# Kernel tuning notes

Measured on AMD Instinct MI355X. Metric: run time of the kernel, lower is better.

The kernel has to match this reference:

```python
import jax, jax.numpy as jnp
import numpy as np

TYPE_PANEL, TYPE_DIALOG, TYPE_CHAR = 1, 2, 3
NUM_ELEMS = 64  # max element index per type (panel count cap per page)
B, S, D = 8, 4096, 768
NPC, NDS = 4, 4  # num_panel_classes, num_dialog_shapes


def setup_inputs() -> dict:
    key = jax.random.key(0)
    ks = jax.random.split(key, 16)
    w = lambda k, shp: jax.random.normal(k, shp, dtype=jnp.float32) * 0.02
    return {
        "element_types": jax.random.randint(ks[0], (B, S), 0, 4, dtype=jnp.int32),
        "element_indices": jax.random.randint(ks[1], (B, S), 0, NUM_ELEMS, dtype=jnp.int32),
        "parent_panel_indices": jax.random.randint(ks[2], (B, S), 0, NUM_ELEMS, dtype=jnp.int32),
        "style_vector": jax.random.normal(ks[3], (B, 4), dtype=jnp.float32),
        "type_emb": w(ks[4], (4, D)),
        "index_emb": w(ks[5], (NUM_ELEMS, D)),
        "parent_emb": w(ks[6], (NUM_ELEMS, D)),
        "style_w": w(ks[7], (4, D)),
        "style_b": jnp.zeros((D,), jnp.float32),
        "ln_g": jnp.ones((D,), jnp.float32),
        "ln_b": jnp.zeros((D,), jnp.float32),
        "panel_w": w(ks[8], (D, NPC + 4)),
        "panel_b": jnp.zeros((NPC + 4,), jnp.float32),
        "dialog_w": w(ks[9], (2 * D, NDS + 4)),
        "dialog_b": jnp.zeros((NDS + 4,), jnp.float32),
        "char_w": w(ks[10], (2 * D, 4)),
        "char_b": jnp.zeros((4,), jnp.float32),
    }


def reference(element_types, element_indices, parent_panel_indices, style_vector,
              type_emb, index_emb, parent_emb, style_w, style_b, ln_g, ln_b,
              panel_w, panel_b, dialog_w, dialog_b, char_w, char_b):
    Bv, Sv = element_types.shape
    # --- TokenLayoutEncoder: embedding sum + style projection + LayerNorm ---
    x = type_emb[element_types] + index_emb[element_indices] + parent_emb[parent_panel_indices]
    x = x + (style_vector @ style_w + style_b)[:, None, :]
    mu = x.mean(-1, keepdims=True)
    var = ((x - mu) ** 2).mean(-1, keepdims=True)
    feats = (x - mu) * jax.lax.rsqrt(var + 1e-5) * ln_g + ln_b  # (B,S,D)

    # --- vectorized _build_parent_remap: orig panel idx -> kept panel order pos ---
    panel_mask = element_types == TYPE_PANEL                      # (B,S)
    kept = (jnp.cumsum(panel_mask, axis=1) - 1).astype(jnp.int32) # order pos of each panel token
    brow = jnp.arange(Bv, dtype=jnp.int32)[:, None]
    col = jnp.where(panel_mask, element_indices, NUM_ELEMS)       # dummy slot for non-panels
    remap = (jnp.full((Bv, NUM_ELEMS + 1), -1, jnp.int32)
             .at[brow, col].max(kept))[:, :NUM_ELEMS]             # (B, NUM_ELEMS)
    # kept panel order pos -> sequence position (for parent feature gather)
    slot = jnp.where(panel_mask, kept, Sv)
    seq_ids = jnp.broadcast_to(jnp.arange(Sv, dtype=jnp.int32), (Bv, Sv))
    pos_table = (jnp.zeros((Bv, Sv + 1), jnp.int32)
                 .at[brow, slot].set(seq_ids))[:, :Sv]            # (B,S)

    # --- parent_pos per token (DIALOG/CHAR only), -1 otherwise ---
    child_mask = (element_types == TYPE_DIALOG) | (element_types == TYPE_CHAR)
    ppos = jnp.where(child_mask,
                     jnp.take_along_axis(remap, parent_panel_indices, axis=1), -1)
    valid = ppos >= 0
    pseq = jnp.take_along_axis(pos_table, jnp.clip(ppos, 0, Sv - 1), axis=1)
    parent_feats = jnp.take_along_axis(feats, pseq[..., None], axis=1)
    parent_feats = parent_feats * valid[..., None].astype(feats.dtype)
    cat = jnp.concatenate([feats, parent_feats], axis=-1)         # (B,S,2D)

    # --- ParallelPredictionHeads, masked per token type ---
    panel_out = (feats @ panel_w + panel_b) * panel_mask[..., None].astype(feats.dtype)
    dmask = ((element_types == TYPE_DIALOG) & valid)[..., None].astype(feats.dtype)
    cmask = ((element_types == TYPE_CHAR) & valid)[..., None].astype(feats.dtype)
    dialog_out = (cat @ dialog_w + dialog_b) * dmask
    char_out = (cat @ char_w + char_b) * cmask
    return panel_out, dialog_out, char_out
```

## Files before the change

### kernel.cpp

```cpp
#include <hip/hip_runtime.h>

#define NB 8
#define NS 4096
#define ND 768

#define WPACK_F4 6528

#define MAIN_LDS_F4 3648

typedef float4 f4;

static __device__ __forceinline__ f4 ld4(const float* __restrict__ p, int i) {
    return ((const f4*)p)[i];
}

static __device__ __forceinline__ void dot4(float& acc, const f4& a, const f4& w) {
    acc = fmaf(a.x, w.x, acc);
    acc = fmaf(a.y, w.y, acc);
    acc = fmaf(a.z, w.z, acc);
    acc = fmaf(a.w, w.w, acc);
}

__global__ __launch_bounds__(256) void lp_pre(
    const int* __restrict__ et, const int* __restrict__ ei,
    const float* __restrict__ sv, const float* __restrict__ sw,
    const float* __restrict__ sb,
    const float* __restrict__ pw, const float* __restrict__ dw,
    const float* __restrict__ cw,
    const float* __restrict__ lng, const float* __restrict__ lnb,
    int* __restrict__ table, int* __restrict__ cnt, int* __restrict__ lists,
    float* __restrict__ sprj, float* __restrict__ wpack)
{
    const int bx = blockIdx.x;
    if (bx < 128) {
        const int lane = threadIdx.x & 63;
        const int t = bx * 256 + threadIdx.x;
        const int b = t >> 12;
        const int s = t & (NS - 1);
        const int type = et[t];
        if (type == 1) atomicMax(&table[b * 64 + ei[t]], s + 1);
        #pragma unroll
        for (int role = 0; role < 3; ++role) {
            const int want = (type == role + 1);
            unsigned long long m = __ballot(want);
            if (want) {
                int ldr = __ffsll(m) - 1;
                int base = 0;
                if (lane == ldr) base = atomicAdd(&cnt[role * 8 + b], (int)__popcll(m));
                base = __shfl(base, ldr, 64);
                int pos = (int)__popcll(m & ((1ull << lane) - 1));
                lists[(role * 8 + b) * 4096 + base + pos] = s;
            }
        }
    } else if (bx < 130) {
        const int lane = threadIdx.x & 63;
        const int b = (bx - 128) * 4 + (threadIdx.x >> 6);
        const float sv0 = sv[b*4+0], sv1 = sv[b*4+1], sv2 = sv[b*4+2], sv3 = sv[b*4+3];
        #pragma unroll
        for (int g = 0; g < 3; ++g) {
            int i = g*64 + lane;
            f4 w0 = ld4(sw, i), w1 = ld4(sw, 192+i), w2 = ld4(sw, 384+i), w3 = ld4(sw, 576+i);
            f4 bb = ld4(sb, i);
            f4 r;
            r.x = bb.x + sv0*w0.x + sv1*w1.x + sv2*w2.x + sv3*w3.x;
            r.y = bb.y + sv0*w0.y + sv1*w1.y + sv2*w2.y + sv3*w3.y;
            r.z = bb.z + sv0*w0.z + sv1*w1.z + sv2*w2.z + sv3*w3.z;
            r.w = bb.w + sv0*w0.w + sv1*w1.w + sv2*w2.w + sv3*w3.w;
            ((f4*)(sprj + b*ND))[i] = r;
        }
    } else {
        const int q = (bx - 130) * 256 + threadIdx.x;
        if (q >= WPACK_F4) return;
        f4 r;
        if (q < 1536) {
            int o = q / 192, i = q - o * 192, d0 = 4 * i;
            r.x = pw[(d0+0)*8 + o];
            r.y = pw[(d0+1)*8 + o];
            r.z = pw[(d0+2)*8 + o];
            r.w = pw[(d0+3)*8 + o];
        } else if (q < 4608) {
            int u = q - 1536;
            int o = u / 384, i = u - o * 384;
            int d0 = (i < 192) ? 4*i : 768 + 4*(i - 192);
            r.x = dw[(d0+0)*8 + o];
            r.y = dw[(d0+1)*8 + o];
            r.z = dw[(d0+2)*8 + o];
            r.w = dw[(d0+3)*8 + o];
        } else if (q < 6144) {
            int u = q - 4608;
            int o = u / 384, i = u - o * 384;
            int d0 = (i < 192) ? 4*i : 768 + 4*(i - 192);
            r.x = cw[(d0+0)*4 + o];
            r.y = cw[(d0+1)*4 + o];
            r.z = cw[(d0+2)*4 + o];
            r.w = cw[(d0+3)*4 + o];
        } else if (q < 6336) {
            r = ld4(lng, q - 6144);
        } else {
            r = ld4(lnb, q - 6336);
        }
        ((f4*)wpack)[q] = r;
    }
}

__global__ __launch_bounds__(256) void lp_parent(
    const int* __restrict__ ei, const int* __restrict__ ppi,
    const float* __restrict__ temb, const float* __restrict__ iemb,
    const float* __restrict__ pemb, const float* __restrict__ lng,
    const float* __restrict__ lnb,
    const int* __restrict__ table, const float* __restrict__ sprj,
    float* __restrict__ pfeat)
{
    const int lane = threadIdx.x & 63;
    const int slot = blockIdx.x * 4 + (threadIdx.x >> 6);
    const int b = slot >> 6;
    const int pp = table[slot] - 1;
    if (pp < 0) return;
    const int ptok = b * NS + pp;
    const int pei = ei[ptok], pppi = ppi[ptok];
    const float* ie = iemb + pei * ND;
    const float* pe = pemb + pppi * ND;
    const float* sp = sprj + b * ND;

    f4 x[3]; float s1 = 0.f, sq = 0.f;
    #pragma unroll
    for (int g = 0; g < 3; ++g) {
        int i = g*64 + lane;
        f4 a = ld4(temb + ND, i), c = ld4(ie, i), d = ld4(pe, i), s = ld4(sp, i);
        f4 v;
        v.x = a.x + c.x + d.x + s.x;
        v.y = a.y + c.y + d.y + s.y;
        v.z = a.z + c.z + d.z + s.z;
        v.w = a.w + c.w + d.w + s.w;
        x[g] = v;
        s1 += v.x + v.y + v.z + v.w;
        sq = fmaf(v.x, v.x, sq);
        sq = fmaf(v.y, v.y, sq);
        sq = fmaf(v.z, v.z, sq);
        sq = fmaf(v.w, v.w, sq);
    }
    #pragma unroll
    for (int k = 32; k >= 1; k >>= 1) {
        s1 += __shfl_xor(s1, k, 64);
        sq += __shfl_xor(sq, k, 64);
    }
    float mu = s1 * (1.f/ND);
    float rs = rsqrtf(sq * (1.f/ND) - mu * mu + 1e-5f);
    float c0 = -mu * rs;
    float* dst = pfeat + (size_t)slot * ND;
    #pragma unroll
    for (int g = 0; g < 3; ++g) {
        int i = g*64 + lane;
        f4 gg = ld4(lng, i), bb = ld4(lnb, i);
        f4 v = x[g], xn;
        xn.x = fmaf(v.x, rs, c0); v.x = fmaf(xn.x, gg.x, bb.x);
        xn.y = fmaf(v.y, rs, c0); v.y = fmaf(xn.y, gg.y, bb.y);
        xn.z = fmaf(v.z, rs, c0); v.z = fmaf(xn.z, gg.z, bb.z);
        xn.w = fmaf(v.w, rs, c0); v.w = fmaf(xn.w, gg.w, bb.w);
        ((f4*)dst)[i] = v;
    }
}

__global__ __launch_bounds__(1024) void lp_main(
    const int* __restrict__ ei, const int* __restrict__ ppi,
    const float* __restrict__ temb, const float* __restrict__ iemb,
    const float* __restrict__ pemb,
    const float* __restrict__ pb, const float* __restrict__ db,
    const float* __restrict__ cb,
    const int* __restrict__ table, const int* __restrict__ cnt,
    const int* __restrict__ lists, const float* __restrict__ sprj,
    const float* __restrict__ wpack, const float* __restrict__ pfeat,
    float* __restrict__ out)
{
    __shared__ f4 S[MAIN_LDS_F4];
    const int tid = threadIdx.x;
    const int lane = tid & 63;
    const int wid = tid >> 6;
    const int bx = blockIdx.x;
    const int b = bx >> 6;
    const int r = bx & 63;

    int role, ridx, nb, wbase, wcnt;
    if (r < 16)      { role = 0; ridx = r;      nb = 16; wbase = 0;    wcnt = 1536; }
    else if (r < 48) { role = 1; ridx = r - 16; nb = 32; wbase = 1536; wcnt = 3072; }
    else             { role = 2; ridx = r - 48; nb = 16; wbase = 4608; wcnt = 1536; }

    const f4* wsrc = (const f4*)wpack;
    for (int i = tid; i < wcnt; i += 1024) S[i] = wsrc[wbase + i];
    if (tid < 384) S[3072 + tid] = wsrc[6144 + tid];
    if (tid < 192) S[3456 + tid] = ((const f4*)(sprj + b * ND))[tid];
    __syncthreads();

    const int n = cnt[role * 8 + b];
    const int* lst = lists + (role * 8 + b) * 4096;
    const int tb = b * NS;
    const int step = nb * 16;
    const float* te = temb + (role + 1) * ND;

    for (int i = ridx * 16 + wid; i < n; i += step) {
        const int s = lst[i];
        const int t = tb + s;
        const int my_ei = ei[t], my_ppi = ppi[t];

        int pp = 0;
        if (role != 0) {
            pp = table[b * 64 + my_ppi] - 1;
            if (pp < 0) continue;
        }

        const float* ie = iemb + my_ei * ND;
        const float* pe = pemb + my_ppi * ND;

        f4 x[3];
        float s1 = 0.f, sq = 0.f;
        #pragma unroll
        for (int g = 0; g < 3; ++g) {
            int ii = g * 64 + lane;
            f4 a = ld4(te, ii), c = ld4(ie, ii), d = ld4(pe, ii);
            f4 sp = S[3456 + ii];
            f4 v;
            v.x = a.x + c.x + d.x + sp.x;
            v.y = a.y + c.y + d.y + sp.y;
            v.z = a.z + c.z + d.z + sp.z;
            v.w = a.w + c.w + d.w + sp.w;
            x[g] = v;
            s1 += v.x + v.y + v.z + v.w;
            sq = fmaf(v.x, v.x, sq);
            sq = fmaf(v.y, v.y, sq);
            sq = fmaf(v.z, v.z, sq);
            sq = fmaf(v.w, v.w, sq);
        }
        #pragma unroll
        for (int k = 32; k >= 1; k >>= 1) {
            s1 += __shfl_xor(s1, k, 64);
            sq += __shfl_xor(sq, k, 64);
        }
        float mu = s1 * (1.f / ND);
        float rs = rsqrtf(sq * (1.f / ND) - mu * mu + 1e-5f);
        float c0 = -mu * rs;
        #pragma unroll
        for (int g = 0; g < 3; ++g) {
            int ii = g * 64 + lane;
            f4 gg = S[3072 + ii], bb = S[3264 + ii];
            f4 v = x[g], xn;
            xn.x = fmaf(v.x, rs, c0); v.x = fmaf(xn.x, gg.x, bb.x);
            xn.y = fmaf(v.y, rs, c0); v.y = fmaf(xn.y, gg.y, bb.y);
            xn.z = fmaf(v.z, rs, c0); v.z = fmaf(xn.z, gg.z, bb.z);
            xn.w = fmaf(v.w, rs, c0); v.w = fmaf(xn.w, gg.w, bb.w);
            x[g] = v;
        }

        if (role == 0) {
            float acc[8];
            #pragma unroll
            for (int o = 0; o < 8; ++o) acc[o] = 0.f;
            #pragma unroll
            for (int g = 0; g < 3; ++g) {
                int ii = g * 64 + lane;
                #pragma unroll
                for (int o = 0; o < 8; ++o)
                    dot4(acc[o], x[g], S[o * 192 + ii]);
            }
            #pragma unroll
            for (int k = 32; k >= 1; k >>= 1) {
                #pragma unroll
                for (int o = 0; o < 8; ++o)
                    acc[o] += __shfl_xor(acc[o], k, 64);
            }
            if (lane == 0) {
                f4 r0, r1;
                r0.x = acc[0] + pb[0]; r0.y = acc[1] + pb[1];
                r0.z = acc[2] + pb[2]; r0.w = acc[3] + pb[3];
                r1.x = acc[4] + pb[4]; r1.y = acc[5] + pb[5];
                r1.z = acc[6] + pb[6]; r1.w = acc[7] + pb[7];
                f4* op = (f4*)(out + (size_t)t * 8);
                op[0] = r0; op[1] = r1;
            }
        } else {
            const float* pfr = pfeat + (size_t)(b * 64 + my_ppi) * ND;
            if (role == 1) {
                float acc[8];
                #pragma unroll
                for (int o = 0; o < 8; ++o) acc[o] = 0.f;
                #pragma unroll
                for (int g = 0; g < 3; ++g) {
                    int ii = g * 64 + lane;
                    #pragma unroll
                    for (int o = 0; o < 8; ++o)
                        dot4(acc[o], x[g], S[o * 384 + ii]);
                }
                #pragma unroll
                for (int g = 0; g < 3; ++g)
                    x[g] = ld4(pfr, g * 64 + lane);
                #pragma unroll
                for (int g = 0; g < 3; ++g) {
                    int ii = g * 64 + lane;
                    #pragma unroll
                    for (int o = 0; o < 8; ++o)
                        dot4(acc[o], x[g], S[o * 384 + 192 + ii]);
                }
                #pragma unroll
                for (int k = 32; k >= 1; k >>= 1) {
                    #pragma unroll
                    for (int o = 0; o < 8; ++o)
                        acc[o] += __shfl_xor(acc[o], k, 64);
                }
                if (lane == 0) {
                    f4 r0, r1;
                    r0.x = acc[0] + db[0]; r0.y = acc[1] + db[1];
                    r0.z = acc[2] + db[2]; r0.w = acc[3] + db[3];
                    r1.x = acc[4] + db[4]; r1.y = acc[5] + db[5];
                    r1.z = acc[6] + db[6]; r1.w = acc[7] + db[7];
                    f4* od = (f4*)(out + (size_t)NB * NS * 8 + (size_t)t * 8);
                    od[0] = r0; od[1] = r1;
                }
            } else {
                float acc[4];
                #pragma unroll
                for (int o = 0; o < 4; ++o) acc[o] = 0.f;
                #pragma unroll
                for (int g = 0; g < 3; ++g) {
                    int ii = g * 64 + lane;
                    #pragma unroll
                    for (int o = 0; o < 4; ++o)
                        dot4(acc[o], x[g], S[o * 384 + ii]);
                }
                #pragma unroll
                for (int g = 0; g < 3; ++g)
                    x[g] = ld4(pfr, g * 64 + lane);
                #pragma unroll
                for (int g = 0; g < 3; ++g) {
                    int ii = g * 64 + lane;
                    #pragma unroll
                    for (int o = 0; o < 4; ++o)
                        dot4(acc[o], x[g], S[o * 384 + 192 + ii]);
                }
                #pragma unroll
                for (int k = 32; k >= 1; k >>= 1) {
                    #pragma unroll
                    for (int o = 0; o < 4; ++o)
                        acc[o] += __shfl_xor(acc[o], k, 64);
                }
                if (lane == 0) {
                    f4 r0;
                    r0.x = acc[0] + cb[0]; r0.y = acc[1] + cb[1];
                    r0.z = acc[2] + cb[2]; r0.w = acc[3] + cb[3];
                    ((f4*)(out + (size_t)NB * NS * 16 + (size_t)t * 4))[0] = r0;
                }
            }
        }
    }
}

extern "C" void kernel_launch(void* const* d_in, const int* in_sizes, int n_in,
                              void* d_out, int out_size, void* d_ws, size_t ws_size,
                              hipStream_t stream) {
    const int* et  = (const int*)d_in[0];
    const int* ei  = (const int*)d_in[1];
    const int* ppi = (const int*)d_in[2];
    const float* sv   = (const float*)d_in[3];
    const float* temb = (const float*)d_in[4];
    const float* iemb = (const float*)d_in[5];
    const float* pemb = (const float*)d_in[6];
    const float* sw   = (const float*)d_in[7];
    const float* sb   = (const float*)d_in[8];
    const float* lng  = (const float*)d_in[9];
    const float* lnb  = (const float*)d_in[10];
    const float* pw   = (const float*)d_in[11];
    const float* pb   = (const float*)d_in[12];
    const float* dw   = (const float*)d_in[13];
    const float* db   = (const float*)d_in[14];
    const float* cw   = (const float*)d_in[15];
    const float* cbp  = (const float*)d_in[16];
    float* out = (float*)d_out;

    int*   table = (int*)d_ws;
    int*   cnt   = (int*)((char*)d_ws + 2048);
    float* sprj  = (float*)((char*)d_ws + 4096);
    float* wpack = (float*)((char*)d_ws + 32768);
    int*   lists = (int*)((char*)d_ws + 137216);
    float* pfeat = (float*)((char*)d_ws + 532480);

    hipMemsetAsync(d_ws, 0, 2144, stream);
    hipMemsetAsync(d_out, 0, out_size, stream);

    lp_pre<<<156, 256, 0, stream>>>(et, ei, sv, sw, sb, pw, dw, cw, lng, lnb,
                                    table, cnt, lists, sprj, wpack);
    lp_parent<<<128, 256, 0, stream>>>(ei, ppi, temb, iemb, pemb, lng, lnb,
                                       table, sprj, pfeat);
    lp_main<<<512, 1024, 0, stream>>>(ei, ppi, temb, iemb, pemb,
                                      pb, db, cbp,
                                      table, cnt, lists, sprj, wpack, pfeat,
                                      out);
}
```

Baseline: 152.1 us.

## Replace compacted per-role token lists with direct strided token scan in main kernel

Drops the ballot/atomic list compaction and per-role counters in the pre-pass. The main kernel now scans tokens directly: each block pair owns a contiguous chunk of 128 tokens, one block handling panel and char tokens and the other dialog tokens, with the next token's metadata prefetched. The table is initialised to -1 with memset and stores the raw position, which removes the off-by-one encoding. This cuts atomics and list traffic, but waves now idle on tokens that belong to the other role, so load balance depends on the type mix.

Measured after the change: 139.8 us. 8.1% less time.

```diff
diff --git a/kernel.cpp b/kernel.cpp
--- a/kernel.cpp
+++ b/kernel.cpp
@@ -28,29 +28,15 @@
     const float* __restrict__ pw, const float* __restrict__ dw,
     const float* __restrict__ cw,
     const float* __restrict__ lng, const float* __restrict__ lnb,
-    int* __restrict__ table, int* __restrict__ cnt, int* __restrict__ lists,
-    float* __restrict__ sprj, float* __restrict__ wpack)
+    int* __restrict__ table, float* __restrict__ sprj,
+    float* __restrict__ wpack)
 {
     const int bx = blockIdx.x;
     if (bx < 128) {
-        const int lane = threadIdx.x & 63;
-        const int t = bx * 256 + threadIdx.x;
-        const int b = t >> 12;
-        const int s = t & (NS - 1);
-        const int type = et[t];
-        if (type == 1) atomicMax(&table[b * 64 + ei[t]], s + 1);
-        #pragma unroll
-        for (int role = 0; role < 3; ++role) {
-            const int want = (type == role + 1);
-            unsigned long long m = __ballot(want);
-            if (want) {
-                int ldr = __ffsll(m) - 1;
-                int base = 0;
-                if (lane == ldr) base = atomicAdd(&cnt[role * 8 + b], (int)__popcll(m));
-                base = __shfl(base, ldr, 64);
-                int pos = (int)__popcll(m & ((1ull << lane) - 1));
-                lists[(role * 8 + b) * 4096 + base + pos] = s;
-            }
+        int t = bx * 256 + threadIdx.x;
+        if (et[t] == 1) {
+            int b = t >> 12;
+            atomicMax(&table[b * 64 + ei[t]], t & (NS - 1));
         }
     } else if (bx < 130) {
         const int lane = threadIdx.x & 63;
@@ -114,7 +100,7 @@
     const int lane = threadIdx.x & 63;
     const int slot = blockIdx.x * 4 + (threadIdx.x >> 6);
     const int b = slot >> 6;
-    const int pp = table[slot] - 1;
+    const int pp = table[slot];
     if (pp < 0) return;
     const int ptok = b * NS + pp;
     const int pei = ei[ptok], pppi = ppi[ptok];
@@ -162,13 +148,12 @@
 }
 
 __global__ __launch_bounds__(1024) void lp_main(
-    const int* __restrict__ ei, const int* __restrict__ ppi,
+    const int* __restrict__ et, const int* __restrict__ ei, const int* __restrict__ ppi,
     const float* __restrict__ temb, const float* __restrict__ iemb,
     const float* __restrict__ pemb,
     const float* __restrict__ pb, const float* __restrict__ db,
     const float* __restrict__ cb,
-    const int* __restrict__ table, const int* __restrict__ cnt,
-    const int* __restrict__ lists, const float* __restrict__ sprj,
+    const int* __restrict__ table, const float* __restrict__ sprj,
     const float* __restrict__ wpack, const float* __restrict__ pfeat,
     float* __restrict__ out)
 {
@@ -177,178 +162,183 @@
     const int lane = tid & 63;
     const int wid = tid >> 6;
     const int bx = blockIdx.x;
-    const int b = bx >> 6;
-    const int r = bx & 63;
-
-    int role, ridx, nb, wbase, wcnt;
-    if (r < 16)      { role = 0; ridx = r;      nb = 16; wbase = 0;    wcnt = 1536; }
-    else if (r < 48) { role = 1; ridx = r - 16; nb = 32; wbase = 1536; wcnt = 3072; }
-    else             { role = 2; ridx = r - 48; nb = 16; wbase = 4608; wcnt = 1536; }
+    const int pair = bx >> 1;
+    const int role = bx & 1;
+    const int b = pair >> 5;
 
     const f4* wsrc = (const f4*)wpack;
-    for (int i = tid; i < wcnt; i += 1024) S[i] = wsrc[wbase + i];
+    if (role == 0) {
+        for (int i = tid; i < 1536; i += 1024) {
+            S[i] = wsrc[i];
+            S[1536 + i] = wsrc[4608 + i];
+        }
+    } else {
+        for (int i = tid; i < 3072; i += 1024)
+            S[i] = wsrc[1536 + i];
+    }
     if (tid < 384) S[3072 + tid] = wsrc[6144 + tid];
     if (tid < 192) S[3456 + tid] = ((const f4*)(sprj + b * ND))[tid];
     __syncthreads();
 
-    const int n = cnt[role * 8 + b];
-    const int* lst = lists + (role * 8 + b) * 4096;
-    const int tb = b * NS;
-    const int step = nb * 16;
-    const float* te = temb + (role + 1) * ND;
-
-    for (int i = ridx * 16 + wid; i < n; i += step) {
-        const int s = lst[i];
-        const int t = tb + s;
-        const int my_ei = ei[t], my_ppi = ppi[t];
-
-        int pp = 0;
-        if (role != 0) {
-            pp = table[b * 64 + my_ppi] - 1;
-            if (pp < 0) continue;
-        }
-
-        const float* ie = iemb + my_ei * ND;
-        const float* pe = pemb + my_ppi * ND;
-
-        f4 x[3];
-        float s1 = 0.f, sq = 0.f;
-        #pragma unroll
-        for (int g = 0; g < 3; ++g) {
-            int ii = g * 64 + lane;
-            f4 a = ld4(te, ii), c = ld4(ie, ii), d = ld4(pe, ii);
-            f4 sp = S[3456 + ii];
-            f4 v;
-            v.x = a.x + c.x + d.x + sp.x;
-            v.y = a.y + c.y + d.y + sp.y;
-            v.z = a.z + c.z + d.z + sp.z;
-            v.w = a.w + c.w + d.w + sp.w;
-            x[g] = v;
-            s1 += v.x + v.y + v.z + v.w;
-            sq = fmaf(v.x, v.x, sq);
-            sq = fmaf(v.y, v.y, sq);
-            sq = fmaf(v.z, v.z, sq);
-            sq = fmaf(v.w, v.w, sq);
-        }
-        #pragma unroll
-        for (int k = 32; k >= 1; k >>= 1) {
-            s1 += __shfl_xor(s1, k, 64);
-            sq += __shfl_xor(sq, k, 64);
-        }
-        float mu = s1 * (1.f / ND);
-        float rs = rsqrtf(sq * (1.f / ND) - mu * mu + 1e-5f);
-        float c0 = -mu * rs;
-        #pragma unroll
-        for (int g = 0; g < 3; ++g) {
-            int ii = g * 64 + lane;
-            f4 gg = S[3072 + ii], bb = S[3264 + ii];
-            f4 v = x[g], xn;
-            xn.x = fmaf(v.x, rs, c0); v.x = fmaf(xn.x, gg.x, bb.x);
-            xn.y = fmaf(v.y, rs, c0); v.y = fmaf(xn.y, gg.y, bb.y);
-            xn.z = fmaf(v.z, rs, c0); v.z = fmaf(xn.z, gg.z, bb.z);
-            xn.w = fmaf(v.w, rs, c0); v.w = fmaf(xn.w, gg.w, bb.w);
-            x[g] = v;
-        }
-
-        if (role == 0) {
-            float acc[8];
-            #pragma unroll
-            for (int o = 0; o < 8; ++o) acc[o] = 0.f;
-            #pragma unroll
-            for (int g = 0; g < 3; ++g) {
-                int ii = g * 64 + lane;
-                #pragma unroll
-                for (int o = 0; o < 8; ++o)
-                    dot4(acc[o], x[g], S[o * 192 + ii]);
-            }
-            #pragma unroll
-            for (int k = 32; k >= 1; k >>= 1) {
-                #pragma unroll
-                for (int o = 0; o < 8; ++o)
-                    acc[o] += __shfl_xor(acc[o], k, 64);
-            }
-            if (lane == 0) {
-                f4 r0, r1;
-                r0.x = acc[0] + pb[0]; r0.y = acc[1] + pb[1];
-                r0.z = acc[2] + pb[2]; r0.w = acc[3] + pb[3];
-                r1.x = acc[4] + pb[4]; r1.y = acc[5] + pb[5];
-                r1.z = acc[6] + pb[6]; r1.w = acc[7] + pb[7];
-                f4* op = (f4*)(out + (size_t)t * 8);
-                op[0] = r0; op[1] = r1;
-            }
-        } else {
-            const float* pfr = pfeat + (size_t)(b * 64 + my_ppi) * ND;
-            if (role == 1) {
-                float acc[8];
-                #pragma unroll
-                for (int o = 0; o < 8; ++o) acc[o] = 0.f;
+    int t = pair * 128 + wid;
+    int type = et[t], my_ei = ei[t], my_ppi = ppi[t];
+
+    for (int r = 0; r < 8; ++r) {
+        const int tn = t + 16;
+        int type_n = 0, ei_n = 0, ppi_n = 0;
+        if (r < 7) { type_n = et[tn]; ei_n = ei[tn]; ppi_n = ppi[tn]; }
+
+        const bool mine = role ? (type == 2) : (type == 1 || type == 3);
+        if (mine) {
+            int pp = -1;
+            if (type != 1) pp = table[b * 64 + my_ppi];
+
+            if (type == 1 || pp >= 0) {
+                const float* te = temb + type * ND;
+                const float* ie = iemb + my_ei * ND;
+                const float* pe = pemb + my_ppi * ND;
+
+                f4 x[3];
+                float s1 = 0.f, sq = 0.f;
                 #pragma unroll
                 for (int g = 0; g < 3; ++g) {
                     int ii = g * 64 + lane;
-                    #pragma unroll
-                    for (int o = 0; o < 8; ++o)
-                        dot4(acc[o], x[g], S[o * 384 + ii]);
+                    f4 a = ld4(te, ii), c = ld4(ie, ii), d = ld4(pe, ii);
+                    f4 sp = S[3456 + ii];
+                    f4 v;
+                    v.x = a.x + c.x + d.x + sp.x;
+                    v.y = a.y + c.y + d.y + sp.y;
+                    v.z = a.z + c.z + d.z + sp.z;
+                    v.w = a.w + c.w + d.w + sp.w;
+                    x[g] = v;
+                    s1 += v.x + v.y + v.z + v.w;
+                    sq = fmaf(v.x, v.x, sq);
+                    sq = fmaf(v.y, v.y, sq);
+                    sq = fmaf(v.z, v.z, sq);
+                    sq = fmaf(v.w, v.w, sq);
                 }
                 #pragma unroll
-                for (int g = 0; g < 3; ++g)
-                    x[g] = ld4(pfr, g * 64 + lane);
+                for (int k = 32; k >= 1; k >>= 1) {
+                    s1 += __shfl_xor(s1, k, 64);
+                    sq += __shfl_xor(sq, k, 64);
+                }
+                float mu = s1 * (1.f / ND);
+                float rs = rsqrtf(sq * (1.f / ND) - mu * mu + 1e-5f);
+                float c0 = -mu * rs;
                 #pragma unroll
                 for (int g = 0; g < 3; ++g) {
                     int ii = g * 64 + lane;
-                    #pragma unroll
-                    for (int o = 0; o < 8; ++o)
-                        dot4(acc[o], x[g], S[o * 384 + 192 + ii]);
+                    f4 gg = S[3072 + ii], bb = S[3264 + ii];
+                    f4 v = x[g], xn;
+                    xn.x = fmaf(v.x, rs, c0); v.x = fmaf(xn.x, gg.x, bb.x);
+                    xn.y = fmaf(v.y, rs, c0); v.y = fmaf(xn.y, gg.y, bb.y);
+                    xn.z = fmaf(v.z, rs, c0); v.z = fmaf(xn.z, gg.z, bb.z);
+                    xn.w = fmaf(v.w, rs, c0); v.w = fmaf(xn.w, gg.w, bb.w);
+                    x[g] = v;
                 }
-                #pragma unroll
-                for (int k = 32; k >= 1; k >>= 1) {
-                    #pragma unroll
-                    for (int o = 0; o < 8; ++o)
-                        acc[o] += __shfl_xor(acc[o], k, 64);
-                }
-                if (lane == 0) {
-                    f4 r0, r1;
-                    r0.x = acc[0] + db[0]; r0.y = acc[1] + db[1];
-                    r0.z = acc[2] + db[2]; r0.w = acc[3] + db[3];
-                    r1.x = acc[4] + db[4]; r1.y = acc[5] + db[5];
-                    r1.z = acc[6] + db[6]; r1.w = acc[7] + db[7];
-                    f4* od = (f4*)(out + (size_t)NB * NS * 8 + (size_t)t * 8);
-                    od[0] = r0; od[1] = r1;
-                }
-            } else {
-                float acc[4];
-                #pragma unroll
-                for (int o = 0; o < 4; ++o) acc[o] = 0.f;
-                #pragma unroll
-                for (int g = 0; g < 3; ++g) {
-                    int ii = g * 64 + lane;
-                    #pragma unroll
-                    for (int o = 0; o < 4; ++o)
-                        dot4(acc[o], x[g], S[o * 384 + ii]);
-                }
-                #pragma unroll
-                for (int g = 0; g < 3; ++g)
-                    x[g] = ld4(pfr, g * 64 + lane);
-                #pragma unroll
-                for (int g = 0; g < 3; ++g) {
-                    int ii = g * 64 + lane;
-                    #pragma unroll
-                    for (int o = 0; o < 4; ++o)
-                        dot4(acc[o], x[g], S[o * 384 + 192 + ii]);
-                }
-                #pragma unroll
-                for (int k = 32; k >= 1; k >>= 1) {
-                    #pragma unroll
-                    for (int o = 0; o < 4; ++o)
-                        acc[o] += __shfl_xor(acc[o], k, 64);
-                }
-                if (lane == 0) {
-                    f4 r0;
-                    r0.x = acc[0] + cb[0]; r0.y = acc[1] + cb[1];
-                    r0.z = acc[2] + cb[2]; r0.w = acc[3] + cb[3];
-                    ((f4*)(out + (size_t)NB * NS * 16 + (size_t)t * 4))[0] = r0;
+
+                if (type == 1) {
+                    float acc[8];
+                    #pragma unroll
+                    for (int o = 0; o < 8; ++o) acc[o] = 0.f;
+                    #pragma unroll
+                    for (int g = 0; g < 3; ++g) {
+                        int ii = g * 64 + lane;
+                        #pragma unroll
+                        for (int o = 0; o < 8; ++o)
+                            dot4(acc[o], x[g], S[o * 192 + ii]);
+                    }
+                    #pragma unroll
+                    for (int k = 32; k >= 1; k >>= 1) {
+                        #pragma unroll
+                        for (int o = 0; o < 8; ++o)
+                            acc[o] += __shfl_xor(acc[o], k, 64);
+                    }
+                    if (lane == 0) {
+                        f4 r0, r1;
+                        r0.x = acc[0] + pb[0]; r0.y = acc[1] + pb[1];
+                        r0.z = acc[2] + pb[2]; r0.w = acc[3] + pb[3];
+                        r1.x = acc[4] + pb[4]; r1.y = acc[5] + pb[5];
+                        r1.z = acc[6] + pb[6]; r1.w = acc[7] + pb[7];
+                        f4* op = (f4*)(out + (size_t)t * 8);
+                        op[0] = r0; op[1] = r1;
+                    }
+                } else if (type == 2) {
+                    const float* pfr = pfeat + (size_t)(b * 64 + my_ppi) * ND;
+                    float acc[8];
+                    #pragma unroll
+                    for (int o = 0; o < 8; ++o) acc[o] = 0.f;
+                    #pragma unroll
+                    for (int g = 0; g < 3; ++g) {
+                        int ii = g * 64 + lane;
+                        #pragma unroll
+                        for (int o = 0; o < 8; ++o)
+                            dot4(acc[o], x[g], S[o * 384 + ii]);
+                    }
+                    #pragma unroll
+                    for (int g = 0; g < 3; ++g)
+                        x[g] = ld4(pfr, g * 64 + lane);
+                    #pragma unroll
+                    for (int g = 0; g < 3; ++g) {
+                        int ii = g * 64 + lane;
+                        #pragma unroll
+                        for (int o = 0; o < 8; ++o)
+                            dot4(acc[o], x[g], S[o * 384 + 192 + ii]);
+                    }
+                    #pragma unroll
+                    for (int k = 32; k >= 1; k >>= 1) {
+                        #pragma unroll
+                        for (int o = 0; o < 8; ++o)
+                            acc[o] += __shfl_xor(acc[o], k, 64);
+                    }
+                    if (lane == 0) {
+                        f4 r0, r1;
+                        r0.x = acc[0] + db[0]; r0.y = acc[1] + db[1];
+                        r0.z = acc[2] + db[2]; r0.w = acc[3] + db[3];
+                        r1.x = acc[4] + db[4]; r1.y = acc[5] + db[5];
+                        r1.z = acc[6] + db[6]; r1.w = acc[7] + db[7];
+                        f4* od = (f4*)(out + (size_t)NB * NS * 8 + (size_t)t * 8);
+                        od[0] = r0; od[1] = r1;
+                    }
+                } else {
+                    const float* pfr = pfeat + (size_t)(b * 64 + my_ppi) * ND;
+                    float acc[4];
+                    #pragma unroll
+                    for (int o = 0; o < 4; ++o) acc[o] = 0.f;
+                    #pragma unroll
+                    for (int g = 0; g < 3; ++g) {
+                        int ii = g * 64 + lane;
+                        #pragma unroll
+                        for (int o = 0; o < 4; ++o)
+                            dot4(acc[o], x[g], S[1536 + o * 384 + ii]);
+                    }
+                    #pragma unroll
+                    for (int g = 0; g < 3; ++g)
+                        x[g] = ld4(pfr, g * 64 + lane);
+                    #pragma unroll
+                    for (int g = 0; g < 3; ++g) {
+                        int ii = g * 64 + lane;
+                        #pragma unroll
+                        for (int o = 0; o < 4; ++o)
+                            dot4(acc[o], x[g], S[1536 + o * 384 + 192 + ii]);
+                    }
+                    #pragma unroll
+                    for (int k = 32; k >= 1; k >>= 1) {
+                        #pragma unroll
+                        for (int o = 0; o < 4; ++o)
+                            acc[o] += __shfl_xor(acc[o], k, 64);
+                    }
+                    if (lane == 0) {
+                        f4 r0;
+                        r0.x = acc[0] + cb[0]; r0.y = acc[1] + cb[1];
+                        r0.z = acc[2] + cb[2]; r0.w = acc[3] + cb[3];
+                        ((f4*)(out + (size_t)NB * NS * 16 + (size_t)t * 4))[0] = r0;
+                    }
                 }
             }
         }
+
+        t = tn; type = type_n; my_ei = ei_n; my_ppi = ppi_n;
     }
 }
 
@@ -375,21 +365,18 @@
     float* out = (float*)d_out;
 
     int*   table = (int*)d_ws;
-    int*   cnt   = (int*)((char*)d_ws + 2048);
     float* sprj  = (float*)((char*)d_ws + 4096);
     float* wpack = (float*)((char*)d_ws + 32768);
-    int*   lists = (int*)((char*)d_ws + 137216);
-    float* pfeat = (float*)((char*)d_ws + 532480);
-
-    hipMemsetAsync(d_ws, 0, 2144, stream);
+    float* pfeat = (float*)((char*)d_ws + 32768 + WPACK_F4 * 16);
+
+    hipMemsetAsync(table, 0xFF, NB * 64 * sizeof(int), stream);
     hipMemsetAsync(d_out, 0, out_size, stream);
 
     lp_pre<<<156, 256, 0, stream>>>(et, ei, sv, sw, sb, pw, dw, cw, lng, lnb,
-                                    table, cnt, lists, sprj, wpack);
+                                    table, sprj, wpack);
     lp_parent<<<128, 256, 0, stream>>>(ei, ppi, temb, iemb, pemb, lng, lnb,
                                        table, sprj, pfeat);
-    lp_main<<<512, 1024, 0, stream>>>(ei, ppi, temb, iemb, pemb,
+    lp_main<<<512, 1024, 0, stream>>>(et, ei, ppi, temb, iemb, pemb,
                                       pb, db, cbp,
-                                      table, cnt, lists, sprj, wpack, pfeat,
-                                      out);
-}
+                                      table, sprj, wpack, pfeat, out);
+}
```
